# Kernel optimization log

Hardware: AMD Instinct MI355X
Metric: run time of the kernel (lower is better)

The kernel has to match this reference:

```python
import jax, jax.numpy as jnp
import numpy as np

B, T, IN, H, NH = 64, 512, 1024, 1024, 4
HD = H // NH  # head_dim = 256
NG = 3        # gates: z (update), r (reset), n (candidate)


def setup_inputs() -> dict:
    key = jax.random.key(0)
    k1, k2, k3, k4, k5 = jax.random.split(key, 5)
    inp = jax.random.normal(k1, (B, T, IN), dtype=jnp.float32)
    # nn.Linear(input_size, 3*hidden_size): weight [3H, IN], bias [3H]
    W = jax.random.normal(k2, (IN, NG * H), dtype=jnp.float32) / np.sqrt(IN)
    bW = jax.random.normal(k3, (NG * H,), dtype=jnp.float32) * 0.02
    # recurrent R: [num_heads, head_dim_in, num_gates, head_dim_out], std=1/sqrt(head_dim)
    R = jax.random.normal(k4, (NH, HD, NG, HD), dtype=jnp.float32) / np.sqrt(HD)
    b = jax.random.normal(k5, (NH, NG, HD), dtype=jnp.float32)
    return {"input": inp, "W": W, "bW": bW, "R": R, "b": b}


def _gru_scan(Wx, R, b, h0):
    # Wx: [T, B, NH, NG, HD], h0: [B, NH, HD]
    def step(h, wx):
        # recurrent gate preactivations: Ry[b,h,g,o] = sum_i h[b,h,i] R[h,i,g,o]
        ry = jnp.einsum('bhi,higo->bhgo', h, R)
        z = jax.nn.sigmoid(wx[:, :, 0] + ry[:, :, 0] + b[:, 0])
        r = jax.nn.sigmoid(wx[:, :, 1] + ry[:, :, 1] + b[:, 1])
        n = jnp.tanh(wx[:, :, 2] + r * ry[:, :, 2] + b[:, 2])
        h_new = z * h + (1.0 - z) * n
        return h_new, h_new

    h_last, hs = jax.lax.scan(step, h0, Wx)
    return hs, h_last  # hs: [T, B, NH, HD]


def reference(input, W, bW, R, b):
    bs, sl = input.shape[0], input.shape[1]
    # input projection for all timesteps at once
    Wx = input @ W + bW                               # [B, T, NG*H]
    Wx = Wx.reshape(bs, sl, NG, NH, HD)
    Wx = jnp.transpose(Wx, (1, 0, 3, 2, 4))           # [T, B, NH, NG, HD]
    h0 = jnp.zeros((bs, NH, HD), dtype=input.dtype)
    hs, h_last = _gru_scan(Wx, R, b, h0)
    h = jnp.transpose(hs, (1, 0, 2, 3)).reshape(bs, sl, H)   # [B, T, H]
    hn = h_last.reshape(1, bs, H)                             # [num_layers=1, B, H]
    return h, hn
```

## Files before the change

### kernel.cpp

```cpp
#include <hip/hip_runtime.h>
#include <hip/hip_fp16.h>


typedef _Float16 f16x8 __attribute__((ext_vector_type(8)));
typedef float    f32x4 __attribute__((ext_vector_type(4)));

#define AS1 __attribute__((address_space(1)))
#define AS3 __attribute__((address_space(3)))

__device__ __forceinline__ void async_ld16(const void* g, void* l) {
    __builtin_amdgcn_global_load_lds((const AS1 void*)g, (AS3 void*)l, 16, 0, 0);
}

__device__ __forceinline__ float sigmoidf_(float x) {
    return 1.f / (1.f + __expf(-x));
}
__device__ __forceinline__ float tanhf_(float x) {
    float e = __expf(-2.f * fabsf(x));
    float r = (1.f - e) / (1.f + e);
    return copysignf(r, x);
}

__global__ __launch_bounds__(256) void cast_to_f16(const float* __restrict__ in,
                                                   _Float16* __restrict__ out, int n8) {
    int i = blockIdx.x * 256 + threadIdx.x;
    if (i >= n8) return;
    const float4* p = (const float4*)in;
    float4 a = p[2 * i], b = p[2 * i + 1];
    f16x8 r;
    r[0] = (_Float16)a.x; r[1] = (_Float16)a.y; r[2] = (_Float16)a.z; r[3] = (_Float16)a.w;
    r[4] = (_Float16)b.x; r[5] = (_Float16)b.y; r[6] = (_Float16)b.z; r[7] = (_Float16)b.w;
    *(f16x8*)(out + (size_t)i * 8) = r;
}

__global__ __launch_bounds__(256) void transpose_cast(const float* __restrict__ W,
                                                      _Float16* __restrict__ WT) {
    __shared__ float tile[32][33];
    const int tx = threadIdx.x, ty = threadIdx.y;
    const int n0 = blockIdx.x * 32, k0 = blockIdx.y * 32;
#pragma unroll
    for (int j = 0; j < 32; j += 8)
        tile[ty + j][tx] = W[(size_t)(k0 + ty + j) * 3072 + n0 + tx];
    __syncthreads();
#pragma unroll
    for (int j = 0; j < 32; j += 8)
        WT[(size_t)(n0 + ty + j) * 1024 + k0 + tx] = (_Float16)tile[tx][ty + j];
}

__global__ __launch_bounds__(256) void gemm_wx(const _Float16* __restrict__ A,
                                               const _Float16* __restrict__ BT,
                                               const float* __restrict__ bW,
                                               const float* __restrict__ bR,
                                               float* __restrict__ Wx) {
    __shared__ _Float16 As[128 * 32];
    __shared__ _Float16 Bs[128 * 32];
    const int tid  = threadIdx.x;
    const int wave = tid >> 6, lane = tid & 63;
    const int m0 = blockIdx.y * 128, n0 = blockIdx.x * 128;
    const int wm = (wave >> 1) * 64, wn = (wave & 1) * 64;
    const int r16 = lane & 15, kq = lane >> 4;

    f32x4 acc[4][4];
#pragma unroll
    for (int m = 0; m < 4; m++)
#pragma unroll
        for (int n = 0; n < 4; n++) acc[m][n] = (f32x4){0.f, 0.f, 0.f, 0.f};

    const int srow = wave * 32 + (lane >> 2);
    const int scol = (lane & 3) * 8;

    for (int kt = 0; kt < 32; kt++) {
        const int k0 = kt * 32;
#pragma unroll
        for (int j = 0; j < 2; j++) {
            async_ld16(A  + (size_t)(m0 + srow + j * 16) * 1024 + k0 + scol,
                       As + (wave * 32 + j * 16) * 32);
            async_ld16(BT + (size_t)(n0 + srow + j * 16) * 1024 + k0 + scol,
                       Bs + (wave * 32 + j * 16) * 32);
        }
        __syncthreads();
        f16x8 af[4], bf[4];
#pragma unroll
        for (int m = 0; m < 4; m++) af[m] = *(const f16x8*)(As + (wm + m * 16 + r16) * 32 + kq * 8);
#pragma unroll
        for (int n = 0; n < 4; n++) bf[n] = *(const f16x8*)(Bs + (wn + n * 16 + r16) * 32 + kq * 8);
#pragma unroll
        for (int m = 0; m < 4; m++)
#pragma unroll
            for (int n = 0; n < 4; n++)
                acc[m][n] = __builtin_amdgcn_mfma_f32_16x16x32_f16(af[m], bf[n], acc[m][n], 0, 0, 0);
        __syncthreads();
    }

#pragma unroll
    for (int m = 0; m < 4; m++) {
        const int row0 = m0 + wm + m * 16 + (lane >> 4) * 4;
#pragma unroll
        for (int n = 0; n < 4; n++) {
            const int col  = n0 + wn + n * 16 + r16;
            const int g    = col >> 10, head = (col >> 8) & 3, o = col & 255;
            const float bias = bW[col] + bR[head * 768 + g * 256 + o];
#pragma unroll
            for (int q = 0; q < 4; q++) {
                const int rr = row0 + q;
                const int t = rr & 511, bb = rr >> 9;
                Wx[(((size_t)t * 64 + bb) * 12 + head * 3 + g) * 256 + o] = acc[m][n][q] + bias;
            }
        }
    }
}

__global__ __launch_bounds__(512) void scan_mfma(const float* __restrict__ R,
                                                 const float* __restrict__ Wx,
                                                 float* __restrict__ out) {
    __shared__ _Float16 Rbuf[3 * 256 * 40];
    __shared__ _Float16 h16[2 * 256];

    const int bx = blockIdx.x;
    const int head = bx >> 6, b = bx & 63;
    const int t0 = threadIdx.x;
    const int w = t0 >> 6, l = t0 & 63;
    const int c = l & 15, kq = l >> 4;
    const int o0 = w * 32;

    f16x8 Bf[3][2][7];
#pragma unroll
    for (int kt = 0; kt < 8; kt++) {
        __syncthreads();
        for (int idx = t0; idx < 32 * 768; idx += 512) {
            const int i2 = idx >> 8 >> 1 >> 0;
            const int ii = idx / 768;
            const int rem = idx - ii * 768;
            const int g = rem >> 8, o = rem & 255;
            Rbuf[(g * 256 + o) * 40 + ii] =
                (_Float16)R[(((size_t)head * 256 + kt * 32 + ii) * 3 + g) * 256 + o];
            (void)i2;
        }
        __syncthreads();
        if (kt < 7) {
#pragma unroll
            for (int g = 0; g < 3; g++)
#pragma unroll
                for (int ot = 0; ot < 2; ot++)
                    Bf[g][ot][kt] =
                        *(const f16x8*)(Rbuf + ((size_t)(g * 256 + o0 + ot * 16 + c)) * 40 + kq * 8);
        }
    }

    if (t0 < 512) { h16[t0] = (_Float16)0.f; }

    float hprev[2] = {0.f, 0.f};
    float wxc[3][2];
#pragma unroll
    for (int g = 0; g < 3; g++)
#pragma unroll
        for (int o2 = 0; o2 < 2; o2++)
            wxc[g][o2] = Wx[(((size_t)0 * 64 + b) * 12 + head * 3 + g) * 256 + o0 + o2 * 16 + c];
    __syncthreads();

    float* outb = out + ((size_t)b * 512) * 1024 + head * 256;
    int cur = 0;

    for (int t = 0; t < 512; t++) {
        f32x4 acc[3][2];
#pragma unroll
        for (int g = 0; g < 3; g++)
#pragma unroll
            for (int ot = 0; ot < 2; ot++) acc[g][ot] = (f32x4){0.f, 0.f, 0.f, 0.f};

#pragma unroll
        for (int kt = 0; kt < 7; kt++) {
            const f16x8 Af = *(const f16x8*)(h16 + cur * 256 + kt * 32 + kq * 8);
#pragma unroll
            for (int g = 0; g < 3; g++)
#pragma unroll
                for (int ot = 0; ot < 2; ot++)
                    acc[g][ot] = __builtin_amdgcn_mfma_f32_16x16x32_f16(Af, Bf[g][ot][kt],
                                                                        acc[g][ot], 0, 0, 0);
        }
        {
            const f16x8 Af = *(const f16x8*)(h16 + cur * 256 + 7 * 32 + kq * 8);
#pragma unroll
            for (int g = 0; g < 3; g++)
#pragma unroll
                for (int ot = 0; ot < 2; ot++) {
                    const f16x8 Bs =
                        *(const f16x8*)(Rbuf + ((size_t)(g * 256 + o0 + ot * 16 + c)) * 40 + kq * 8);
                    acc[g][ot] = __builtin_amdgcn_mfma_f32_16x16x32_f16(Af, Bs,
                                                                        acc[g][ot], 0, 0, 0);
                }
        }

        float wxn[3][2];
        if (t < 511) {
#pragma unroll
            for (int g = 0; g < 3; g++)
#pragma unroll
                for (int o2 = 0; o2 < 2; o2++)
                    wxn[g][o2] = Wx[(((size_t)(t + 1) * 64 + b) * 12 + head * 3 + g) * 256 +
                                    o0 + o2 * 16 + c];
        } else {
            wxn[0][0] = wxn[0][1] = wxn[1][0] = wxn[1][1] = wxn[2][0] = wxn[2][1] = 0.f;
        }

#pragma unroll
        for (int o2 = 0; o2 < 2; o2++) {
            const float z = sigmoidf_(wxc[0][o2] + acc[0][o2][0]);
            const float r = sigmoidf_(wxc[1][o2] + acc[1][o2][0]);
            const float n = tanhf_(wxc[2][o2] + r * acc[2][o2][0]);
            const float h = z * hprev[o2] + (1.f - z) * n;
            hprev[o2] = h;
            if (kq == 0) {
                outb[(size_t)t * 1024 + o0 + o2 * 16 + c] = h;
                h16[(cur ^ 1) * 256 + o0 + o2 * 16 + c] = (_Float16)h;
            }
        }
#pragma unroll
        for (int g = 0; g < 3; g++)
#pragma unroll
            for (int o2 = 0; o2 < 2; o2++) wxc[g][o2] = wxn[g][o2];

        __syncthreads();
        cur ^= 1;
    }
}

__global__ __launch_bounds__(256) void copy_hn(float* __restrict__ out) {
    const int idx = blockIdx.x * 256 + threadIdx.x;
    out[(size_t)64 * 512 * 1024 + idx] =
        out[((size_t)(idx >> 10) * 512 + 511) * 1024 + (idx & 1023)];
}

extern "C" void kernel_launch(void* const* d_in, const int* in_sizes, int n_in,
                              void* d_out, int out_size, void* d_ws, size_t ws_size,
                              hipStream_t stream) {
    (void)in_sizes; (void)n_in; (void)out_size; (void)ws_size;
    const float* inp = (const float*)d_in[0];
    const float* W   = (const float*)d_in[1];
    const float* bW  = (const float*)d_in[2];
    const float* R   = (const float*)d_in[3];
    const float* bR  = (const float*)d_in[4];
    float* out = (float*)d_out;

    _Float16* A16 = (_Float16*)d_ws;
    _Float16* WT  = (_Float16*)((char*)d_ws + 67108864);
    float*    Wx  = (float*)((char*)d_ws + 73400320);

    cast_to_f16<<<16384, 256, 0, stream>>>(inp, A16, 4194304);
    transpose_cast<<<dim3(96, 32), dim3(32, 8), 0, stream>>>(W, WT);
    gemm_wx<<<dim3(24, 256), 256, 0, stream>>>(A16, WT, bW, bR, Wx);
    scan_mfma<<<256, 512, 0, stream>>>(R, Wx, out);
    copy_hn<<<256, 256, 0, stream>>>(out);
}
```

Baseline: 1.057 ms.

## Store Wx in fp16, prefetch two steps ahead in scan, fold hn write

The gate preactivation buffer Wx is now written by the GEMM and read by the scan in fp16 rather than fp32, halving that intermediate traffic. The scan loop is unrolled by two with double-buffered register prefetch of Wx two timesteps ahead, so global load latency can overlap the recurrent MFMA step. The final hidden state is written directly at t=511, which removes the separate copy_hn launch. Storing Wx in fp16 adds rounding error to the gate inputs.

Measured after the change: 1.168 ms. 10.5% more time.

```diff
diff --git a/kernel.cpp b/kernel.cpp
--- a/kernel.cpp
+++ b/kernel.cpp
@@ -51,7 +51,7 @@
                                                const _Float16* __restrict__ BT,
                                                const float* __restrict__ bW,
                                                const float* __restrict__ bR,
-                                               float* __restrict__ Wx) {
+                                               _Float16* __restrict__ Wx) {
     __shared__ _Float16 As[128 * 32];
     __shared__ _Float16 Bs[128 * 32];
     const int tid  = threadIdx.x;
@@ -104,14 +104,15 @@
             for (int q = 0; q < 4; q++) {
                 const int rr = row0 + q;
                 const int t = rr & 511, bb = rr >> 9;
-                Wx[(((size_t)t * 64 + bb) * 12 + head * 3 + g) * 256 + o] = acc[m][n][q] + bias;
+                Wx[(((size_t)t * 64 + bb) * 12 + head * 3 + g) * 256 + o] =
+                    (_Float16)(acc[m][n][q] + bias);
             }
         }
     }
 }
 
 __global__ __launch_bounds__(512) void scan_mfma(const float* __restrict__ R,
-                                                 const float* __restrict__ Wx,
+                                                 const _Float16* __restrict__ Wx,
                                                  float* __restrict__ out) {
     __shared__ _Float16 Rbuf[3 * 256 * 40];
     __shared__ _Float16 h16[2 * 256];
@@ -128,13 +129,11 @@
     for (int kt = 0; kt < 8; kt++) {
         __syncthreads();
         for (int idx = t0; idx < 32 * 768; idx += 512) {
-            const int i2 = idx >> 8 >> 1 >> 0;
             const int ii = idx / 768;
             const int rem = idx - ii * 768;
             const int g = rem >> 8, o = rem & 255;
             Rbuf[(g * 256 + o) * 40 + ii] =
                 (_Float16)R[(((size_t)head * 256 + kt * 32 + ii) * 3 + g) * 256 + o];
-            (void)i2;
         }
         __syncthreads();
         if (kt < 7) {
@@ -147,30 +146,37 @@
         }
     }
 
-    if (t0 < 512) { h16[t0] = (_Float16)0.f; }
+    h16[t0] = (_Float16)0.f;
 
     float hprev[2] = {0.f, 0.f};
-    float wxc[3][2];
-#pragma unroll
-    for (int g = 0; g < 3; g++)
-#pragma unroll
-        for (int o2 = 0; o2 < 2; o2++)
-            wxc[g][o2] = Wx[(((size_t)0 * 64 + b) * 12 + head * 3 + g) * 256 + o0 + o2 * 16 + c];
+    float* outb = out + ((size_t)b * 512) * 1024 + head * 256;
+    float* hnp  = out + (size_t)64 * 512 * 1024 + b * 1024 + head * 256;
+
+    const _Float16* wxbase = Wx + ((size_t)b * 12 + head * 3) * 256 + o0 + c;
+    _Float16 wxA[6], wxB[6];
+#define WXLD(dst, ts)                                              \
+    {                                                              \
+        const _Float16* wp = wxbase + (size_t)(ts) * 196608;       \
+        dst[0] = wp[0];   dst[1] = wp[16];                         \
+        dst[2] = wp[256]; dst[3] = wp[272];                        \
+        dst[4] = wp[512]; dst[5] = wp[528];                        \
+    }
+    WXLD(wxA, 0);
+    WXLD(wxB, 1);
     __syncthreads();
 
-    float* outb = out + ((size_t)b * 512) * 1024 + head * 256;
     int cur = 0;
-
-    for (int t = 0; t < 512; t++) {
+    auto dostep = [&](int t, const _Float16* wxc) {
         f32x4 acc[3][2];
 #pragma unroll
         for (int g = 0; g < 3; g++)
 #pragma unroll
             for (int ot = 0; ot < 2; ot++) acc[g][ot] = (f32x4){0.f, 0.f, 0.f, 0.f};
 
+        const _Float16* hc = h16 + cur * 256;
 #pragma unroll
         for (int kt = 0; kt < 7; kt++) {
-            const f16x8 Af = *(const f16x8*)(h16 + cur * 256 + kt * 32 + kq * 8);
+            const f16x8 Af = *(const f16x8*)(hc + kt * 32 + kq * 8);
 #pragma unroll
             for (int g = 0; g < 3; g++)
 #pragma unroll
@@ -179,7 +185,7 @@
                                                                         acc[g][ot], 0, 0, 0);
         }
         {
-            const f16x8 Af = *(const f16x8*)(h16 + cur * 256 + 7 * 32 + kq * 8);
+            const f16x8 Af = *(const f16x8*)(hc + 7 * 32 + kq * 8);
 #pragma unroll
             for (int g = 0; g < 3; g++)
 #pragma unroll
@@ -190,45 +196,33 @@
                                                                         acc[g][ot], 0, 0, 0);
                 }
         }
-
-        float wxn[3][2];
-        if (t < 511) {
-#pragma unroll
-            for (int g = 0; g < 3; g++)
-#pragma unroll
-                for (int o2 = 0; o2 < 2; o2++)
-                    wxn[g][o2] = Wx[(((size_t)(t + 1) * 64 + b) * 12 + head * 3 + g) * 256 +
-                                    o0 + o2 * 16 + c];
-        } else {
-            wxn[0][0] = wxn[0][1] = wxn[1][0] = wxn[1][1] = wxn[2][0] = wxn[2][1] = 0.f;
-        }
-
+        _Float16* hw = h16 + (cur ^ 1) * 256;
 #pragma unroll
         for (int o2 = 0; o2 < 2; o2++) {
-            const float z = sigmoidf_(wxc[0][o2] + acc[0][o2][0]);
-            const float r = sigmoidf_(wxc[1][o2] + acc[1][o2][0]);
-            const float n = tanhf_(wxc[2][o2] + r * acc[2][o2][0]);
+            const float z = sigmoidf_((float)wxc[0 * 2 + o2] + acc[0][o2][0]);
+            const float r = sigmoidf_((float)wxc[1 * 2 + o2] + acc[1][o2][0]);
+            const float n = tanhf_((float)wxc[2 * 2 + o2] + r * acc[2][o2][0]);
             const float h = z * hprev[o2] + (1.f - z) * n;
             hprev[o2] = h;
             if (kq == 0) {
                 outb[(size_t)t * 1024 + o0 + o2 * 16 + c] = h;
-                h16[(cur ^ 1) * 256 + o0 + o2 * 16 + c] = (_Float16)h;
+                hw[o0 + o2 * 16 + c] = (_Float16)h;
+                if (t == 511) hnp[o0 + o2 * 16 + c] = h;
             }
         }
-#pragma unroll
-        for (int g = 0; g < 3; g++)
-#pragma unroll
-            for (int o2 = 0; o2 < 2; o2++) wxc[g][o2] = wxn[g][o2];
-
+    };
+
+    for (int tt = 0; tt < 512; tt += 2) {
+        dostep(tt, wxA);
+        if (tt + 2 < 512) WXLD(wxA, tt + 2);
         __syncthreads();
         cur ^= 1;
-    }
-}
-
-__global__ __launch_bounds__(256) void copy_hn(float* __restrict__ out) {
-    const int idx = blockIdx.x * 256 + threadIdx.x;
-    out[(size_t)64 * 512 * 1024 + idx] =
-        out[((size_t)(idx >> 10) * 512 + 511) * 1024 + (idx & 1023)];
+        dostep(tt + 1, wxB);
+        if (tt + 3 < 512) WXLD(wxB, tt + 3);
+        __syncthreads();
+        cur ^= 1;
+    }
+#undef WXLD
 }
 
 extern "C" void kernel_launch(void* const* d_in, const int* in_sizes, int n_in,
@@ -244,11 +238,10 @@
 
     _Float16* A16 = (_Float16*)d_ws;
     _Float16* WT  = (_Float16*)((char*)d_ws + 67108864);
-    float*    Wx  = (float*)((char*)d_ws + 73400320);
+    _Float16* Wx  = (_Float16*)((char*)d_ws + 73400320);
 
     cast_to_f16<<<16384, 256, 0, stream>>>(inp, A16, 4194304);
     transpose_cast<<<dim3(96, 32), dim3(32, 8), 0, stream>>>(W, WT);
     gemm_wx<<<dim3(24, 256), 256, 0, stream>>>(A16, WT, bW, bR, Wx);
     scan_mfma<<<256, 512, 0, stream>>>(R, Wx, out);
-    copy_hn<<<256, 256, 0, stream>>>(out);
-}
+}
```
